# Kernel optimization log

Measured on AMD Instinct MI355X. Metric: run time of the kernel, lower is better.

The kernel has to match this reference:

```python
import jax, jax.numpy as jnp
import numpy as np
import math

HEADS = 12
D_MODEL = 768
D_K = D_MODEL // HEADS


def setup_inputs() -> dict:
    key = jax.random.key(0)
    ks = jax.random.split(key, 11)
    B, S, D = 2, 2048, D_MODEL
    p = 0.02
    return {
        "query": jax.random.normal(ks[0], (B, S, D), jnp.float32),
        "key": jax.random.normal(ks[1], (B, S, D), jnp.float32),
        "value": jax.random.normal(ks[2], (B, S, D), jnp.float32),
        "Wq": jax.random.normal(ks[3], (D, D), jnp.float32) * p,
        "bq": jax.random.normal(ks[4], (D,), jnp.float32) * p,
        "Wk": jax.random.normal(ks[5], (D, D), jnp.float32) * p,
        "bk": jax.random.normal(ks[6], (D,), jnp.float32) * p,
        "Wv": jax.random.normal(ks[7], (D, D), jnp.float32) * p,
        "bv": jax.random.normal(ks[8], (D,), jnp.float32) * p,
        "Wo": jax.random.normal(ks[9], (D, D), jnp.float32) * p,
        "bo": jax.random.normal(ks[10], (D,), jnp.float32) * p,
    }


def reference(query, key, value, Wq, bq, Wk, bk, Wv, bv, Wo, bo):
    B, S, D = query.shape
    scale = 1.0 / math.sqrt(D_K)
    # Linear projections then split into heads: [B,S,H,Dk]
    q = (query @ Wq + bq).reshape(B, S, HEADS, D_K)
    k = (key @ Wk + bk).reshape(B, S, HEADS, D_K)
    v = (value @ Wv + bv).reshape(B, S, HEADS, D_K)
    # Full score tensor [B, i, j, H]
    scores = jnp.einsum('bihd,bjhd->bijh', q, k) * scale
    # Faithful to source: nn.Softmax(dim=1) over [b,i,j,h] -> query axis i
    attn = jax.nn.softmax(scores, axis=1)
    # dropout_prob=0 (inference/deterministic reference)
    x = jnp.einsum('bijh,bjhd->bihd', attn, v).reshape(B, S, D)
    return x @ Wo + bo
```

## Files before the change

### kernel.cpp

```cpp
#include <hip/hip_runtime.h>
#include <stdint.h>

#define HEADS 12
#define DK 64
#define DM 768
#define BT 2
#define SEQ 2048
#define ROWS (BT*SEQ)

typedef __bf16 bf16x4 __attribute__((ext_vector_type(4)));
typedef __bf16 bf16x8 __attribute__((ext_vector_type(8)));
typedef float f32x4 __attribute__((ext_vector_type(4)));

#define SCL2 0.18033688011112042f

__device__ __forceinline__ float exp2fast(float x) {
#if __has_builtin(__builtin_amdgcn_exp2f)
    return __builtin_amdgcn_exp2f(x);
#else
    return exp2f(x);
#endif
}
__device__ __forceinline__ float rcpfast(float x) {
#if __has_builtin(__builtin_amdgcn_rcpf)
    return __builtin_amdgcn_rcpf(x);
#else
    return 1.0f / x;
#endif
}

__device__ __forceinline__ uint16_t f2bf(float f) {
    union { float f; uint32_t u; } v; v.f = f;
    uint32_t u = v.u;
    return (uint16_t)((u + 0x7FFFu + ((u >> 16) & 1u)) >> 16);
}
__device__ __forceinline__ float bf2f(uint16_t u) {
    union { uint32_t u; float f; } v; v.u = ((uint32_t)u) << 16;
    return v.f;
}

union U8 { uint16_t u[8]; bf16x8 v; float4 f; };

__device__ __forceinline__ bf16x8 cat44(bf16x4 lo, bf16x4 hi) {
    bf16x8 f;
    f[0] = lo[0]; f[1] = lo[1]; f[2] = lo[2]; f[3] = lo[3];
    f[4] = hi[0]; f[5] = hi[1]; f[6] = hi[2]; f[7] = hi[3];
    return f;
}

__device__ __forceinline__ bf16x8 ldfrag(const char* p) {
    bf16x4 lo = *(const bf16x4*)p;
    bf16x4 hi = *(const bf16x4*)(p + 32);
    return cat44(lo, hi);
}

__global__ __launch_bounds__(256) void k_transpose(const float* __restrict__ Wq,
                                                   const float* __restrict__ Wk,
                                                   const float* __restrict__ Wv,
                                                   const float* __restrict__ Wo,
                                                   uint16_t* __restrict__ Wqt,
                                                   uint16_t* __restrict__ Wkt,
                                                   uint16_t* __restrict__ Wvt,
                                                   uint16_t* __restrict__ Wot) {
    __shared__ float t[32][33];
    int z = blockIdx.z;
    const float* W = (z == 0) ? Wq : (z == 1) ? Wk : (z == 2) ? Wv : Wo;
    uint16_t* Wt = (z == 0) ? Wqt : (z == 1) ? Wkt : (z == 2) ? Wvt : Wot;
    int bx = blockIdx.x * 32;
    int by = blockIdx.y * 32;
    int tx = threadIdx.x & 31, ty = threadIdx.x >> 5;
#pragma unroll
    for (int r = 0; r < 32; r += 8)
        t[ty + r][tx] = W[(size_t)(bx + ty + r) * DM + by + tx];
    __syncthreads();
#pragma unroll
    for (int r = 0; r < 32; r += 8)
        Wt[(size_t)(by + ty + r) * DM + bx + tx] = f2bf(t[tx][ty + r]);
}

__global__ __launch_bounds__(256) void k_gemm_qkv(const float* __restrict__ Aq,
                                                  const float* __restrict__ Ak,
                                                  const float* __restrict__ Av,
                                                  const uint16_t* __restrict__ Wt,
                                                  const float* __restrict__ bq,
                                                  const float* __restrict__ bk,
                                                  const float* __restrict__ bv,
                                                  uint16_t* __restrict__ Qm,
                                                  uint16_t* __restrict__ Km,
                                                  uint16_t* __restrict__ VT) {
    __shared__ char smem[2 * 2 * 128 * 80];
    const int z = blockIdx.z;
    const float* A = (z == 0) ? Aq : (z == 1) ? Ak : Av;
    const uint16_t* Bt = Wt + (size_t)z * DM * DM;
    const float* bias = (z == 0) ? bq : (z == 1) ? bk : bv;
    const int tid = threadIdx.x, lane = tid & 63, w = tid >> 6;
    const int q = lane >> 4, r16 = lane & 15;
    const int mtile = blockIdx.y * 128, ntile = blockIdx.x * 128;
    const int wm = (w >> 1) * 64, wn = (w & 1) * 64;
    const int srow = tid >> 1, shalf = tid & 1;
    const float* ap = A + (size_t)(mtile + srow) * DM + shalf * 16;
    const uint16_t* bp = Bt + (size_t)(ntile + srow) * DM + shalf * 16;
    f32x4 acc[4][4] = {};
    float4 ra0 = *(const float4*)(ap + 0);
    float4 ra1 = *(const float4*)(ap + 4);
    float4 ra2 = *(const float4*)(ap + 8);
    float4 ra3 = *(const float4*)(ap + 12);
    float4 rb0 = *(const float4*)(bp + 0);
    float4 rb1 = *(const float4*)((const char*)bp + 16);
    for (int t = 0; t < 24; ++t) {
        char* As = smem + (t & 1) * 20480;
        char* Bs = As + 10240;
        U8 pk0, pk1;
        pk0.u[0] = f2bf(ra0.x); pk0.u[1] = f2bf(ra0.y); pk0.u[2] = f2bf(ra0.z); pk0.u[3] = f2bf(ra0.w);
        pk0.u[4] = f2bf(ra1.x); pk0.u[5] = f2bf(ra1.y); pk0.u[6] = f2bf(ra1.z); pk0.u[7] = f2bf(ra1.w);
        pk1.u[0] = f2bf(ra2.x); pk1.u[1] = f2bf(ra2.y); pk1.u[2] = f2bf(ra2.z); pk1.u[3] = f2bf(ra2.w);
        pk1.u[4] = f2bf(ra3.x); pk1.u[5] = f2bf(ra3.y); pk1.u[6] = f2bf(ra3.z); pk1.u[7] = f2bf(ra3.w);
        *(float4*)(As + srow * 80 + shalf * 32) = pk0.f;
        *(float4*)(As + srow * 80 + shalf * 32 + 16) = pk1.f;
        *(float4*)(Bs + srow * 80 + shalf * 32) = rb0;
        *(float4*)(Bs + srow * 80 + shalf * 32 + 16) = rb1;
        if (t < 23) {
            const float* ap2 = ap + (t + 1) * 32;
            ra0 = *(const float4*)(ap2 + 0);
            ra1 = *(const float4*)(ap2 + 4);
            ra2 = *(const float4*)(ap2 + 8);
            ra3 = *(const float4*)(ap2 + 12);
            const uint16_t* bp2 = bp + (t + 1) * 32;
            rb0 = *(const float4*)bp2;
            rb1 = *(const float4*)((const char*)bp2 + 16);
        }
        __syncthreads();
        bf16x8 af[4], bfr[4];
#pragma unroll
        for (int i = 0; i < 4; i++) {
            af[i] = ldfrag(As + (wm + i * 16 + r16) * 80 + q * 8);
            bfr[i] = ldfrag(Bs + (wn + i * 16 + r16) * 80 + q * 8);
        }
#pragma unroll
        for (int mi = 0; mi < 4; mi++)
#pragma unroll
            for (int ni = 0; ni < 4; ni++)
                acc[mi][ni] = __builtin_amdgcn_mfma_f32_16x16x32_bf16(
                    af[mi], bfr[ni], acc[mi][ni], 0, 0, 0);
    }
    if (z < 2) {
        uint16_t* out = (z == 0) ? Qm : Km;
#pragma unroll
        for (int ni = 0; ni < 4; ni++) {
            int n = ntile + wn + ni * 16 + r16;
            float bv2 = bias[n];
#pragma unroll
            for (int mi = 0; mi < 4; mi++)
#pragma unroll
                for (int r = 0; r < 4; r++) {
                    int m = mtile + wm + mi * 16 + 4 * q + r;
                    out[(size_t)m * DM + n] = f2bf(acc[mi][ni][r] + bv2);
                }
        }
    } else {
#pragma unroll
        for (int ni = 0; ni < 4; ni++) {
            int n = ntile + wn + ni * 16 + r16;
            int h = n >> 6, dk = n & 63;
            float bv2 = bias[n];
#pragma unroll
            for (int mi = 0; mi < 4; mi++) {
                int mbase = mtile + wm + mi * 16 + 4 * q;
                int b = mbase >> 11, s = mbase & 2047;
                ushort4 o;
                o.x = f2bf(acc[mi][ni][0] + bv2);
                o.y = f2bf(acc[mi][ni][1] + bv2);
                o.z = f2bf(acc[mi][ni][2] + bv2);
                o.w = f2bf(acc[mi][ni][3] + bv2);
                *(ushort4*)(VT + ((size_t)((b * HEADS + h) * DK + dk)) * SEQ + s) = o;
            }
        }
    }
}

__global__ __launch_bounds__(256) void k_gemm_o(const uint16_t* __restrict__ A,
                                                const uint16_t* __restrict__ Bt,
                                                const float* __restrict__ bias,
                                                float* __restrict__ C) {
    __shared__ char smem[2 * 2 * 128 * 80];
    const int tid = threadIdx.x, lane = tid & 63, w = tid >> 6;
    const int q = lane >> 4, r16 = lane & 15;
    const int mtile = blockIdx.y * 128, ntile = blockIdx.x * 128;
    const int wm = (w >> 1) * 64, wn = (w & 1) * 64;
    const int srow = tid >> 1, shalf = tid & 1;
    const uint16_t* ap = A + (size_t)(mtile + srow) * DM + shalf * 16;
    const uint16_t* bp = Bt + (size_t)(ntile + srow) * DM + shalf * 16;
    f32x4 acc[4][4] = {};
    float4 ra0 = *(const float4*)ap;
    float4 ra1 = *(const float4*)((const char*)ap + 16);
    float4 rb0 = *(const float4*)bp;
    float4 rb1 = *(const float4*)((const char*)bp + 16);
    for (int t = 0; t < 24; ++t) {
        char* As = smem + (t & 1) * 20480;
        char* Bs = As + 10240;
        *(float4*)(As + srow * 80 + shalf * 32) = ra0;
        *(float4*)(As + srow * 80 + shalf * 32 + 16) = ra1;
        *(float4*)(Bs + srow * 80 + shalf * 32) = rb0;
        *(float4*)(Bs + srow * 80 + shalf * 32 + 16) = rb1;
        if (t < 23) {
            const uint16_t* ap2 = ap + (t + 1) * 32;
            ra0 = *(const float4*)ap2;
            ra1 = *(const float4*)((const char*)ap2 + 16);
            const uint16_t* bp2 = bp + (t + 1) * 32;
            rb0 = *(const float4*)bp2;
            rb1 = *(const float4*)((const char*)bp2 + 16);
        }
        __syncthreads();
        bf16x8 af[4], bfr[4];
#pragma unroll
        for (int i = 0; i < 4; i++) {
            af[i] = ldfrag(As + (wm + i * 16 + r16) * 80 + q * 8);
            bfr[i] = ldfrag(Bs + (wn + i * 16 + r16) * 80 + q * 8);
        }
#pragma unroll
        for (int mi = 0; mi < 4; mi++)
#pragma unroll
            for (int ni = 0; ni < 4; ni++)
                acc[mi][ni] = __builtin_amdgcn_mfma_f32_16x16x32_bf16(
                    af[mi], bfr[ni], acc[mi][ni], 0, 0, 0);
    }
#pragma unroll
    for (int ni = 0; ni < 4; ni++) {
        int n = ntile + wn + ni * 16 + r16;
        float bv = bias[n];
#pragma unroll
        for (int mi = 0; mi < 4; mi++)
#pragma unroll
            for (int r = 0; r < 4; r++) {
                int m = mtile + wm + mi * 16 + 4 * q + r;
                C[(size_t)m * DM + n] = acc[mi][ni][r] + bv;
            }
    }
}

__global__ __launch_bounds__(512, 4) void k_stats(const uint16_t* __restrict__ Qm,
                                                  const uint16_t* __restrict__ Km,
                                                  float* __restrict__ Zbuf) {
    __shared__ char lds[2 * 9216];
    const int tid = threadIdx.x, lane = tid & 63, w = tid >> 6;
    const int q = lane >> 4, r16 = lane & 15;
    const int bh = blockIdx.y, b = bh / HEADS, h = bh % HEADS;
    const int j0 = blockIdx.x * 128 + w * 16;
    bf16x8 kf[2];
    {
        const uint16_t* kp = Km + (size_t)(b * SEQ + j0 + r16) * DM + h * DK + q * 4;
#pragma unroll
        for (int ks = 0; ks < 2; ks++)
            kf[ks] = cat44(*(const bf16x4*)(kp + ks * 32),
                           *(const bf16x4*)(kp + ks * 32 + 16));
    }
    const uint16_t* Qbase = Qm + (size_t)b * SEQ * DM + h * DK;
    const int srow = tid >> 3, sseg = tid & 7;
    float4 rq = *(const float4*)(Qbase + (size_t)srow * DM + sseg * 8);
    float Zs[4] = {0.f, 0.f, 0.f, 0.f};
    for (int t = 0; t < 32; ++t) {
        char* Qs = lds + (t & 1) * 9216;
        *(float4*)(Qs + srow * 144 + sseg * 16) = rq;
        if (t < 31)
            rq = *(const float4*)(Qbase + (size_t)((t + 1) * 64 + srow) * DM + sseg * 8);
        __syncthreads();
        f32x4 st[4] = {};
#pragma unroll
        for (int f = 0; f < 4; f++) {
            bf16x8 qf0 = ldfrag(Qs + (f * 16 + r16) * 144 + q * 8);
            bf16x8 qf1 = ldfrag(Qs + (f * 16 + r16) * 144 + 64 + q * 8);
            st[f] = __builtin_amdgcn_mfma_f32_16x16x32_bf16(kf[0], qf0, st[f], 0, 0, 0);
            st[f] = __builtin_amdgcn_mfma_f32_16x16x32_bf16(kf[1], qf1, st[f], 0, 0, 0);
        }
#pragma unroll
        for (int f = 0; f < 4; f++)
#pragma unroll
            for (int r = 0; r < 4; r++)
                Zs[r] += exp2fast(st[f][r] * SCL2);
    }
#pragma unroll
    for (int r = 0; r < 4; r++) {
        float e = Zs[r];
#pragma unroll
        for (int m = 1; m < 16; m <<= 1) e += __shfl_xor(e, m);
        if (r16 == 0) Zbuf[(size_t)bh * SEQ + j0 + 4 * q + r] = e;
    }
}

__global__ __launch_bounds__(256) void k_vscale(uint16_t* __restrict__ VT,
                                                const float* __restrict__ Zbuf) {
    size_t t = (size_t)blockIdx.x * 256 + threadIdx.x;
    size_t base = t * 8;
    int rowid = (int)(base >> 11);
    int bh = rowid >> 6;
    int s0 = (int)(base & 2047);
    const float* Zp = Zbuf + (size_t)bh * SEQ + s0;
    float4 z0 = *(const float4*)Zp;
    float4 z1 = *(const float4*)(Zp + 4);
    ushort4 a = *(ushort4*)(VT + base);
    ushort4 c = *(ushort4*)(VT + base + 4);
    ushort4 oa, oc;
    oa.x = f2bf(bf2f(a.x) * rcpfast(z0.x));
    oa.y = f2bf(bf2f(a.y) * rcpfast(z0.y));
    oa.z = f2bf(bf2f(a.z) * rcpfast(z0.z));
    oa.w = f2bf(bf2f(a.w) * rcpfast(z0.w));
    oc.x = f2bf(bf2f(c.x) * rcpfast(z1.x));
    oc.y = f2bf(bf2f(c.y) * rcpfast(z1.y));
    oc.z = f2bf(bf2f(c.z) * rcpfast(z1.z));
    oc.w = f2bf(bf2f(c.w) * rcpfast(z1.w));
    *(ushort4*)(VT + base) = oa;
    *(ushort4*)(VT + base + 4) = oc;
}

__global__ __launch_bounds__(512, 4) void k_attn(const uint16_t* __restrict__ Qm,
                                                 const uint16_t* __restrict__ Km,
                                                 const uint16_t* __restrict__ VT,
                                                 uint16_t* __restrict__ Xm) {
    __shared__ char lds[2 * 18432];
    const int tid = threadIdx.x, lane = tid & 63, w = tid >> 6;
    const int q = lane >> 4, r16 = lane & 15;
    const int bh = blockIdx.y, b = bh / HEADS, h = bh % HEADS;
    const int i0 = blockIdx.x * 128 + w * 16;
    const uint16_t* Qbase = Qm + (size_t)b * SEQ * DM + h * DK;
    const uint16_t* Kbase = Km + (size_t)b * SEQ * DM + h * DK;
    const uint16_t* VTbase = VT + (size_t)bh * DK * SEQ;
    bf16x8 qf[2];
    {
        const uint16_t* qp = Qbase + (size_t)(i0 + r16) * DM + q * 4;
#pragma unroll
        for (int ks = 0; ks < 2; ks++)
            qf[ks] = cat44(*(const bf16x4*)(qp + ks * 32),
                           *(const bf16x4*)(qp + ks * 32 + 16));
    }
    const int srow = tid >> 3, sseg = tid & 7;
    float4 rk = *(const float4*)(Kbase + (size_t)srow * DM + sseg * 8);
    float4 rv = *(const float4*)(VTbase + (size_t)srow * SEQ + sseg * 8);
    f32x4 xacc[4] = {};
    for (int t = 0; t < 32; ++t) {
        char* Ks = lds + (t & 1) * 18432;
        char* Vs = Ks + 9216;
        *(float4*)(Ks + srow * 144 + sseg * 16) = rk;
        *(float4*)(Vs + srow * 144 + sseg * 16) = rv;
        if (t < 31) {
            int js = (t + 1) * 64;
            rk = *(const float4*)(Kbase + (size_t)(js + srow) * DM + sseg * 8);
            rv = *(const float4*)(VTbase + (size_t)srow * SEQ + js + sseg * 8);
        }
        __syncthreads();
        f32x4 st[4] = {};
#pragma unroll
        for (int jf = 0; jf < 4; jf++) {
            bf16x8 kf0 = ldfrag(Ks + (jf * 16 + r16) * 144 + q * 8);
            bf16x8 kf1 = ldfrag(Ks + (jf * 16 + r16) * 144 + 64 + q * 8);
            st[jf] = __builtin_amdgcn_mfma_f32_16x16x32_bf16(kf0, qf[0], st[jf], 0, 0, 0);
            st[jf] = __builtin_amdgcn_mfma_f32_16x16x32_bf16(kf1, qf[1], st[jf], 0, 0, 0);
        }
        bf16x8 pb[2];
#pragma unroll
        for (int c = 0; c < 2; c++) {
            U8 t8;
#pragma unroll
            for (int r = 0; r < 4; r++) {
                t8.u[r] = f2bf(exp2fast(st[2 * c][r] * SCL2));
                t8.u[4 + r] = f2bf(exp2fast(st[2 * c + 1][r] * SCL2));
            }
            pb[c] = t8.v;
        }
#pragma unroll
        for (int dc = 0; dc < 4; dc++)
#pragma unroll
            for (int c = 0; c < 2; c++) {
                bf16x8 vf = ldfrag(Vs + (dc * 16 + r16) * 144 + c * 64 + q * 8);
                xacc[dc] = __builtin_amdgcn_mfma_f32_16x16x32_bf16(vf, pb[c], xacc[dc], 0, 0, 0);
            }
    }
    __syncthreads();
    char* xr = lds + w * 2304;
#pragma unroll
    for (int dc = 0; dc < 4; dc++)
#pragma unroll
        for (int r = 0; r < 4; r++)
            *(uint16_t*)(xr + r16 * 136 + (dc * 16 + 4 * q + r) * 2) = f2bf(xacc[dc][r]);
#pragma unroll
    for (int cc = 0; cc < 2; cc++) {
        int c = cc * 64 + lane;
        int row = c >> 3, c16 = c & 7;
        *(float4*)(Xm + (size_t)(b * SEQ + i0 + row) * DM + h * DK + c16 * 8) =
            *(const float4*)(xr + row * 136 + c16 * 16);
    }
}

extern "C" void kernel_launch(void* const* d_in, const int* in_sizes, int n_in,
                              void* d_out, int out_size, void* d_ws, size_t ws_size,
                              hipStream_t stream) {
    const float* query = (const float*)d_in[0];
    const float* key = (const float*)d_in[1];
    const float* value = (const float*)d_in[2];
    const float* Wq = (const float*)d_in[3];
    const float* bq = (const float*)d_in[4];
    const float* Wk = (const float*)d_in[5];
    const float* bk = (const float*)d_in[6];
    const float* Wv = (const float*)d_in[7];
    const float* bv = (const float*)d_in[8];
    const float* Wo = (const float*)d_in[9];
    const float* bo = (const float*)d_in[10];
    float* out = (float*)d_out;
    char* ws = (char*)d_ws;

    const size_t SZ = (size_t)ROWS * DM * 2;
    const size_t WSZ = (size_t)DM * DM * 2;
    uint16_t* Qm = (uint16_t*)(ws + 0 * SZ);
    uint16_t* Km = (uint16_t*)(ws + 1 * SZ);
    uint16_t* VT = (uint16_t*)(ws + 2 * SZ);
    uint16_t* Xm = (uint16_t*)(ws + 3 * SZ);
    uint16_t* Wqt = (uint16_t*)(ws + 4 * SZ);
    uint16_t* Wkt = (uint16_t*)(ws + 4 * SZ + WSZ);
    uint16_t* Wvt = (uint16_t*)(ws + 4 * SZ + 2 * WSZ);
    uint16_t* Wot = (uint16_t*)(ws + 4 * SZ + 3 * WSZ);
    float* Zbuf = (float*)(ws + 4 * SZ + 4 * WSZ);

    k_transpose<<<dim3(24, 24, 4), 256, 0, stream>>>(Wq, Wk, Wv, Wo, Wqt, Wkt, Wvt, Wot);
    k_gemm_qkv<<<dim3(6, 32, 3), 256, 0, stream>>>(query, key, value, Wqt, bq, bk, bv, Qm, Km, VT);
    k_stats<<<dim3(16, 24), 512, 0, stream>>>(Qm, Km, Zbuf);
    k_vscale<<<dim3(1536), 256, 0, stream>>>(VT, Zbuf);
    k_attn<<<dim3(16, 24), 512, 0, stream>>>(Qm, Km, VT, Xm);
    k_gemm_o<<<dim3(6, 32), 256, 0, stream>>>(Xm, Wot, bo, out);
}
```

Measured before the change: 275.9 us.

## Fold softmax normalizer into exponent, drop vscale, enlarge per-wave tiles with LDS DMA

The stats kernel now writes -log2 of the column sums, and the attention kernel adds it inside exp2, so the separate V-scaling pass is gone. Both attention kernels move from 8 waves owning 16 rows each to 2 waves owning 64 rows each. Each K/V fragment loaded from LDS is now reused across four query groups. Tiles are staged with direct global-to-LDS loads into an XOR-swizzled layout instead of going through registers, at the cost of higher register pressure and fewer waves per block.

```diff
diff --git a/kernel.cpp b/kernel.cpp
--- a/kernel.cpp
+++ b/kernel.cpp
@@ -21,11 +21,11 @@
     return exp2f(x);
 #endif
 }
-__device__ __forceinline__ float rcpfast(float x) {
-#if __has_builtin(__builtin_amdgcn_rcpf)
-    return __builtin_amdgcn_rcpf(x);
+__device__ __forceinline__ float log2fast(float x) {
+#if __has_builtin(__builtin_amdgcn_logf)
+    return __builtin_amdgcn_logf(x);
 #else
-    return 1.0f / x;
+    return log2f(x);
 #endif
 }
 
@@ -33,10 +33,6 @@
     union { float f; uint32_t u; } v; v.f = f;
     uint32_t u = v.u;
     return (uint16_t)((u + 0x7FFFu + ((u >> 16) & 1u)) >> 16);
-}
-__device__ __forceinline__ float bf2f(uint16_t u) {
-    union { uint32_t u; float f; } v; v.u = ((uint32_t)u) << 16;
-    return v.f;
 }
 
 union U8 { uint16_t u[8]; bf16x8 v; float4 f; };
@@ -52,6 +48,12 @@
     bf16x4 lo = *(const bf16x4*)p;
     bf16x4 hi = *(const bf16x4*)(p + 32);
     return cat44(lo, hi);
+}
+
+typedef __attribute__((address_space(3))) void lds_vp;
+typedef const __attribute__((address_space(1))) void gbl_vp;
+__device__ __forceinline__ void gload16(const void* g, void* l) {
+    __builtin_amdgcn_global_load_lds((gbl_vp*)g, (lds_vp*)l, 16, 0, 0);
 }
 
 __global__ __launch_bounds__(256) void k_transpose(const float* __restrict__ Wq,
@@ -105,7 +107,7 @@
     float4 ra1 = *(const float4*)(ap + 4);
     float4 ra2 = *(const float4*)(ap + 8);
     float4 ra3 = *(const float4*)(ap + 12);
-    float4 rb0 = *(const float4*)(bp + 0);
+    float4 rb0 = *(const float4*)bp;
     float4 rb1 = *(const float4*)((const char*)bp + 16);
     for (int t = 0; t < 24; ++t) {
         char* As = smem + (t & 1) * 20480;
@@ -238,155 +240,198 @@
     }
 }
 
-__global__ __launch_bounds__(512, 4) void k_stats(const uint16_t* __restrict__ Qm,
+__global__ __launch_bounds__(128, 2) void k_stats(const uint16_t* __restrict__ Qm,
                                                   const uint16_t* __restrict__ Km,
-                                                  float* __restrict__ Zbuf) {
-    __shared__ char lds[2 * 9216];
+                                                  float* __restrict__ L2buf) {
+    __shared__ char lds[2 * 8192];
+    const int tid = threadIdx.x, lane = tid & 63;
+    const int w = tid >> 6;
+    const int q = lane >> 4, r16 = lane & 15;
+    const int bh = blockIdx.y, b = bh / HEADS, h = bh % HEADS;
+    const int j0 = blockIdx.x * 128 + w * 64;
+    const uint16_t* Qbase = Qm + (size_t)b * SEQ * DM + h * DK;
+    bf16x8 kf[4][2];
+#pragma unroll
+    for (int jf = 0; jf < 4; jf++) {
+        const uint16_t* kp = Km + (size_t)(b * SEQ + j0 + jf * 16 + r16) * DM + h * DK + q * 4;
+#pragma unroll
+        for (int ks = 0; ks < 2; ks++)
+            kf[jf][ks] = cat44(*(const bf16x4*)(kp + ks * 32),
+                               *(const bf16x4*)(kp + ks * 32 + 16));
+    }
+    float Zs[4][4] = {};
+#pragma unroll
+    for (int c = 0; c < 4; c++) {
+        int n = c * 128 + tid, row = n >> 3, u = n & 7;
+        gload16(Qbase + (size_t)row * DM + ((u ^ (row & 7)) * 8), lds + n * 16);
+    }
+    for (int t = 0; t < 32; ++t) {
+        asm volatile("s_waitcnt vmcnt(0)" ::: "memory");
+        __builtin_amdgcn_s_barrier();
+        if (t < 31) {
+            char* nb = lds + ((t + 1) & 1) * 8192;
+            int i1 = (t + 1) * 64;
+#pragma unroll
+            for (int c = 0; c < 4; c++) {
+                int n = c * 128 + tid, row = n >> 3, u = n & 7;
+                gload16(Qbase + (size_t)(i1 + row) * DM + ((u ^ (row & 7)) * 8), nb + n * 16);
+            }
+        }
+        const char* Qs = lds + (t & 1) * 8192;
+#pragma unroll
+        for (int f = 0; f < 4; f++) {
+            bf16x8 qfr[2];
+#pragma unroll
+            for (int ks = 0; ks < 2; ks++) {
+                int row = f * 16 + r16;
+                int ulo = (ks * 4 + (q >> 1)) ^ (row & 7);
+                int uhi = (ks * 4 + 2 + (q >> 1)) ^ (row & 7);
+                qfr[ks] = cat44(*(const bf16x4*)(Qs + row * 128 + ulo * 16 + (q & 1) * 8),
+                                *(const bf16x4*)(Qs + row * 128 + uhi * 16 + (q & 1) * 8));
+            }
+            f32x4 st[4] = {};
+#pragma unroll
+            for (int jf = 0; jf < 4; jf++)
+#pragma unroll
+                for (int ks = 0; ks < 2; ks++)
+                    st[jf] = __builtin_amdgcn_mfma_f32_16x16x32_bf16(kf[jf][ks], qfr[ks], st[jf], 0, 0, 0);
+#pragma unroll
+            for (int jf = 0; jf < 4; jf++)
+#pragma unroll
+                for (int r = 0; r < 4; r++)
+                    Zs[jf][r] += exp2fast(st[jf][r] * SCL2);
+        }
+    }
+#pragma unroll
+    for (int jf = 0; jf < 4; jf++)
+#pragma unroll
+        for (int r = 0; r < 4; r++) {
+            float e = Zs[jf][r];
+#pragma unroll
+            for (int m = 1; m < 16; m <<= 1) e += __shfl_xor(e, m);
+            if (r16 == 0)
+                L2buf[(size_t)bh * SEQ + j0 + jf * 16 + 4 * q + r] = -log2fast(e);
+        }
+}
+
+__global__ __launch_bounds__(128, 2) void k_attn(const uint16_t* __restrict__ Qm,
+                                                 const uint16_t* __restrict__ Km,
+                                                 const uint16_t* __restrict__ VT,
+                                                 const float* __restrict__ L2,
+                                                 uint16_t* __restrict__ Xm) {
+    __shared__ char lds[2 * 16384];
     const int tid = threadIdx.x, lane = tid & 63, w = tid >> 6;
     const int q = lane >> 4, r16 = lane & 15;
     const int bh = blockIdx.y, b = bh / HEADS, h = bh % HEADS;
-    const int j0 = blockIdx.x * 128 + w * 16;
-    bf16x8 kf[2];
-    {
-        const uint16_t* kp = Km + (size_t)(b * SEQ + j0 + r16) * DM + h * DK + q * 4;
-#pragma unroll
-        for (int ks = 0; ks < 2; ks++)
-            kf[ks] = cat44(*(const bf16x4*)(kp + ks * 32),
-                           *(const bf16x4*)(kp + ks * 32 + 16));
-    }
-    const uint16_t* Qbase = Qm + (size_t)b * SEQ * DM + h * DK;
-    const int srow = tid >> 3, sseg = tid & 7;
-    float4 rq = *(const float4*)(Qbase + (size_t)srow * DM + sseg * 8);
-    float Zs[4] = {0.f, 0.f, 0.f, 0.f};
-    for (int t = 0; t < 32; ++t) {
-        char* Qs = lds + (t & 1) * 9216;
-        *(float4*)(Qs + srow * 144 + sseg * 16) = rq;
-        if (t < 31)
-            rq = *(const float4*)(Qbase + (size_t)((t + 1) * 64 + srow) * DM + sseg * 8);
-        __syncthreads();
-        f32x4 st[4] = {};
-#pragma unroll
-        for (int f = 0; f < 4; f++) {
-            bf16x8 qf0 = ldfrag(Qs + (f * 16 + r16) * 144 + q * 8);
-            bf16x8 qf1 = ldfrag(Qs + (f * 16 + r16) * 144 + 64 + q * 8);
-            st[f] = __builtin_amdgcn_mfma_f32_16x16x32_bf16(kf[0], qf0, st[f], 0, 0, 0);
-            st[f] = __builtin_amdgcn_mfma_f32_16x16x32_bf16(kf[1], qf1, st[f], 0, 0, 0);
-        }
-#pragma unroll
-        for (int f = 0; f < 4; f++)
-#pragma unroll
-            for (int r = 0; r < 4; r++)
-                Zs[r] += exp2fast(st[f][r] * SCL2);
-    }
-#pragma unroll
-    for (int r = 0; r < 4; r++) {
-        float e = Zs[r];
-#pragma unroll
-        for (int m = 1; m < 16; m <<= 1) e += __shfl_xor(e, m);
-        if (r16 == 0) Zbuf[(size_t)bh * SEQ + j0 + 4 * q + r] = e;
-    }
-}
-
-__global__ __launch_bounds__(256) void k_vscale(uint16_t* __restrict__ VT,
-                                                const float* __restrict__ Zbuf) {
-    size_t t = (size_t)blockIdx.x * 256 + threadIdx.x;
-    size_t base = t * 8;
-    int rowid = (int)(base >> 11);
-    int bh = rowid >> 6;
-    int s0 = (int)(base & 2047);
-    const float* Zp = Zbuf + (size_t)bh * SEQ + s0;
-    float4 z0 = *(const float4*)Zp;
-    float4 z1 = *(const float4*)(Zp + 4);
-    ushort4 a = *(ushort4*)(VT + base);
-    ushort4 c = *(ushort4*)(VT + base + 4);
-    ushort4 oa, oc;
-    oa.x = f2bf(bf2f(a.x) * rcpfast(z0.x));
-    oa.y = f2bf(bf2f(a.y) * rcpfast(z0.y));
-    oa.z = f2bf(bf2f(a.z) * rcpfast(z0.z));
-    oa.w = f2bf(bf2f(a.w) * rcpfast(z0.w));
-    oc.x = f2bf(bf2f(c.x) * rcpfast(z1.x));
-    oc.y = f2bf(bf2f(c.y) * rcpfast(z1.y));
-    oc.z = f2bf(bf2f(c.z) * rcpfast(z1.z));
-    oc.w = f2bf(bf2f(c.w) * rcpfast(z1.w));
-    *(ushort4*)(VT + base) = oa;
-    *(ushort4*)(VT + base + 4) = oc;
-}
-
-__global__ __launch_bounds__(512, 4) void k_attn(const uint16_t* __restrict__ Qm,
-                                                 const uint16_t* __restrict__ Km,
-                                                 const uint16_t* __restrict__ VT,
-                                                 uint16_t* __restrict__ Xm) {
-    __shared__ char lds[2 * 18432];
-    const int tid = threadIdx.x, lane = tid & 63, w = tid >> 6;
-    const int q = lane >> 4, r16 = lane & 15;
-    const int bh = blockIdx.y, b = bh / HEADS, h = bh % HEADS;
-    const int i0 = blockIdx.x * 128 + w * 16;
+    const int i0 = blockIdx.x * 128 + w * 64;
     const uint16_t* Qbase = Qm + (size_t)b * SEQ * DM + h * DK;
     const uint16_t* Kbase = Km + (size_t)b * SEQ * DM + h * DK;
-    const uint16_t* VTbase = VT + (size_t)bh * DK * SEQ;
-    bf16x8 qf[2];
-    {
-        const uint16_t* qp = Qbase + (size_t)(i0 + r16) * DM + q * 4;
+    const uint16_t* VTb = VT + (size_t)bh * DK * SEQ;
+    const float* L2b = L2 + (size_t)bh * SEQ;
+    bf16x8 qf[4][2];
+#pragma unroll
+    for (int ig = 0; ig < 4; ig++) {
+        const uint16_t* qp = Qbase + (size_t)(i0 + ig * 16 + r16) * DM + q * 4;
 #pragma unroll
         for (int ks = 0; ks < 2; ks++)
-            qf[ks] = cat44(*(const bf16x4*)(qp + ks * 32),
-                           *(const bf16x4*)(qp + ks * 32 + 16));
-    }
-    const int srow = tid >> 3, sseg = tid & 7;
-    float4 rk = *(const float4*)(Kbase + (size_t)srow * DM + sseg * 8);
-    float4 rv = *(const float4*)(VTbase + (size_t)srow * SEQ + sseg * 8);
-    f32x4 xacc[4] = {};
+            qf[ig][ks] = cat44(*(const bf16x4*)(qp + ks * 32),
+                               *(const bf16x4*)(qp + ks * 32 + 16));
+    }
+    f32x4 xacc[4][4] = {};
+#pragma unroll
+    for (int c = 0; c < 4; c++) {
+        int n = c * 128 + tid, row = n >> 3, u = n & 7;
+        gload16(Kbase + (size_t)row * DM + ((u ^ (row & 7)) * 8), lds + n * 16);
+        gload16(VTb + (size_t)row * SEQ + ((u ^ (row & 7)) * 8), lds + 8192 + n * 16);
+    }
     for (int t = 0; t < 32; ++t) {
-        char* Ks = lds + (t & 1) * 18432;
-        char* Vs = Ks + 9216;
-        *(float4*)(Ks + srow * 144 + sseg * 16) = rk;
-        *(float4*)(Vs + srow * 144 + sseg * 16) = rv;
+        asm volatile("s_waitcnt vmcnt(0)" ::: "memory");
+        __builtin_amdgcn_s_barrier();
         if (t < 31) {
-            int js = (t + 1) * 64;
-            rk = *(const float4*)(Kbase + (size_t)(js + srow) * DM + sseg * 8);
-            rv = *(const float4*)(VTbase + (size_t)srow * SEQ + js + sseg * 8);
-        }
-        __syncthreads();
-        f32x4 st[4] = {};
+            char* nb = lds + ((t + 1) & 1) * 16384;
+            int js1 = (t + 1) * 64;
+#pragma unroll
+            for (int c = 0; c < 4; c++) {
+                int n = c * 128 + tid, row = n >> 3, u = n & 7;
+                gload16(Kbase + (size_t)(js1 + row) * DM + ((u ^ (row & 7)) * 8), nb + n * 16);
+                gload16(VTb + (size_t)row * SEQ + js1 + ((u ^ (row & 7)) * 8), nb + 8192 + n * 16);
+            }
+        }
+        const char* Ks = lds + (t & 1) * 16384;
+        const char* Vs = Ks + 8192;
+        const int js = t * 64;
+        bf16x8 kf[4][2], vf[4][2];
+#pragma unroll
+        for (int jf = 0; jf < 4; jf++)
+#pragma unroll
+            for (int ks = 0; ks < 2; ks++) {
+                int row = jf * 16 + r16;
+                int ulo = (ks * 4 + (q >> 1)) ^ (row & 7);
+                int uhi = (ks * 4 + 2 + (q >> 1)) ^ (row & 7);
+                kf[jf][ks] = cat44(*(const bf16x4*)(Ks + row * 128 + ulo * 16 + (q & 1) * 8),
+                                   *(const bf16x4*)(Ks + row * 128 + uhi * 16 + (q & 1) * 8));
+            }
+#pragma unroll
+        for (int dc = 0; dc < 4; dc++)
+#pragma unroll
+            for (int c = 0; c < 2; c++) {
+                int row = dc * 16 + r16;
+                int ulo = (c * 4 + (q >> 1)) ^ (row & 7);
+                int uhi = (c * 4 + 2 + (q >> 1)) ^ (row & 7);
+                vf[dc][c] = cat44(*(const bf16x4*)(Vs + row * 128 + ulo * 16 + (q & 1) * 8),
+                                  *(const bf16x4*)(Vs + row * 128 + uhi * 16 + (q & 1) * 8));
+            }
+        float l2v[4][4];
 #pragma unroll
         for (int jf = 0; jf < 4; jf++) {
-            bf16x8 kf0 = ldfrag(Ks + (jf * 16 + r16) * 144 + q * 8);
-            bf16x8 kf1 = ldfrag(Ks + (jf * 16 + r16) * 144 + 64 + q * 8);
-            st[jf] = __builtin_amdgcn_mfma_f32_16x16x32_bf16(kf0, qf[0], st[jf], 0, 0, 0);
-            st[jf] = __builtin_amdgcn_mfma_f32_16x16x32_bf16(kf1, qf[1], st[jf], 0, 0, 0);
-        }
-        bf16x8 pb[2];
-#pragma unroll
-        for (int c = 0; c < 2; c++) {
-            U8 t8;
-#pragma unroll
-            for (int r = 0; r < 4; r++) {
-                t8.u[r] = f2bf(exp2fast(st[2 * c][r] * SCL2));
-                t8.u[4 + r] = f2bf(exp2fast(st[2 * c + 1][r] * SCL2));
-            }
-            pb[c] = t8.v;
-        }
-#pragma unroll
-        for (int dc = 0; dc < 4; dc++)
+            float4 lv = *(const float4*)(L2b + js + jf * 16 + 4 * q);
+            l2v[jf][0] = lv.x; l2v[jf][1] = lv.y; l2v[jf][2] = lv.z; l2v[jf][3] = lv.w;
+        }
+#pragma unroll
+        for (int ig = 0; ig < 4; ig++) {
+            f32x4 st[4] = {};
+#pragma unroll
+            for (int jf = 0; jf < 4; jf++)
+#pragma unroll
+                for (int ks = 0; ks < 2; ks++)
+                    st[jf] = __builtin_amdgcn_mfma_f32_16x16x32_bf16(kf[jf][ks], qf[ig][ks], st[jf], 0, 0, 0);
+            bf16x8 pb[2];
 #pragma unroll
             for (int c = 0; c < 2; c++) {
-                bf16x8 vf = ldfrag(Vs + (dc * 16 + r16) * 144 + c * 64 + q * 8);
-                xacc[dc] = __builtin_amdgcn_mfma_f32_16x16x32_bf16(vf, pb[c], xacc[dc], 0, 0, 0);
-            }
+                U8 t8;
+#pragma unroll
+                for (int r = 0; r < 4; r++) {
+                    t8.u[r]     = f2bf(exp2fast(st[2 * c][r] * SCL2 + l2v[2 * c][r]));
+                    t8.u[4 + r] = f2bf(exp2fast(st[2 * c + 1][r] * SCL2 + l2v[2 * c + 1][r]));
+                }
+                pb[c] = t8.v;
+            }
+#pragma unroll
+            for (int dc = 0; dc < 4; dc++)
+#pragma unroll
+                for (int c = 0; c < 2; c++)
+                    xacc[dc][ig] = __builtin_amdgcn_mfma_f32_16x16x32_bf16(vf[dc][c], pb[c], xacc[dc][ig], 0, 0, 0);
+        }
     }
     __syncthreads();
-    char* xr = lds + w * 2304;
+    char* xr = lds + w * 9216;
 #pragma unroll
     for (int dc = 0; dc < 4; dc++)
 #pragma unroll
-        for (int r = 0; r < 4; r++)
-            *(uint16_t*)(xr + r16 * 136 + (dc * 16 + 4 * q + r) * 2) = f2bf(xacc[dc][r]);
-#pragma unroll
-    for (int cc = 0; cc < 2; cc++) {
-        int c = cc * 64 + lane;
-        int row = c >> 3, c16 = c & 7;
-        *(float4*)(Xm + (size_t)(b * SEQ + i0 + row) * DM + h * DK + c16 * 8) =
-            *(const float4*)(xr + row * 136 + c16 * 16);
+        for (int ig = 0; ig < 4; ig++) {
+            bf16x4 pk;
+            pk[0] = (__bf16)xacc[dc][ig][0];
+            pk[1] = (__bf16)xacc[dc][ig][1];
+            pk[2] = (__bf16)xacc[dc][ig][2];
+            pk[3] = (__bf16)xacc[dc][ig][3];
+            *(bf16x4*)(xr + (ig * 16 + r16) * 144 + (dc * 16 + 4 * q) * 2) = pk;
+        }
+    __syncthreads();
+#pragma unroll
+    for (int rr = 0; rr < 8; rr++) {
+        int row = rr * 8 + (lane >> 3), seg = lane & 7;
+        *(float4*)(Xm + (size_t)(b * SEQ + i0 + row) * DM + h * DK + seg * 8) =
+            *(const float4*)(xr + row * 144 + seg * 16);
     }
 }
 
@@ -417,12 +462,11 @@
     uint16_t* Wkt = (uint16_t*)(ws + 4 * SZ + WSZ);
     uint16_t* Wvt = (uint16_t*)(ws + 4 * SZ + 2 * WSZ);
     uint16_t* Wot = (uint16_t*)(ws + 4 * SZ + 3 * WSZ);
-    float* Zbuf = (float*)(ws + 4 * SZ + 4 * WSZ);
+    float* L2buf = (float*)(ws + 4 * SZ + 4 * WSZ);
 
     k_transpose<<<dim3(24, 24, 4), 256, 0, stream>>>(Wq, Wk, Wv, Wo, Wqt, Wkt, Wvt, Wot);
     k_gemm_qkv<<<dim3(6, 32, 3), 256, 0, stream>>>(query, key, value, Wqt, bq, bk, bv, Qm, Km, VT);
-    k_stats<<<dim3(16, 24), 512, 0, stream>>>(Qm, Km, Zbuf);
-    k_vscale<<<dim3(1536), 256, 0, stream>>>(VT, Zbuf);
-    k_attn<<<dim3(16, 24), 512, 0, stream>>>(Qm, Km, VT, Xm);
+    k_stats<<<dim3(16, 24), 128, 0, stream>>>(Qm, Km, L2buf);
+    k_attn<<<dim3(16, 24), 128, 0, stream>>>(Qm, Km, VT, L2buf, Xm);
     k_gemm_o<<<dim3(6, 32), 256, 0, stream>>>(Xm, Wot, bo, out);
 }
```

New measurement: 296.1 us. 1.07x slower.
